# Kernel optimization log

Hardware: AMD Instinct MI355X
Metric: run time of the kernel (lower is better)

The kernel has to match this reference:

```python
import jax, jax.numpy as jnp
import numpy as np

T, B = 128, 32
E, H, V = 512, 1024, 32000


def setup_inputs() -> dict:
    key = jax.random.key(0)
    ks = jax.random.split(key, 9)
    s = 0.02
    return {
        "inputs": jax.random.randint(ks[0], (T, B), 0, V),
        "encoder_output": jax.random.normal(ks[1], (T, B, H), dtype=jnp.float32),
        "encoder_mask": jnp.ones((T, B), dtype=bool),
        "emb": jax.random.normal(ks[2], (V, E), dtype=jnp.float32) * s,
        "w_ih": jax.random.normal(ks[3], (3 * H, E), dtype=jnp.float32) * s,
        "w_hh": jax.random.normal(ks[4], (3 * H, H), dtype=jnp.float32) * s,
        "b_ih": jax.random.normal(ks[5], (3 * H,), dtype=jnp.float32) * s,
        "b_hh": jax.random.normal(ks[6], (3 * H,), dtype=jnp.float32) * s,
        "out_w": jax.random.normal(ks[7], (V, H), dtype=jnp.float32) * s,
        "out_b": jax.random.normal(ks[8], (V,), dtype=jnp.float32) * s,
    }


def reference(inputs, encoder_output, encoder_mask, emb, w_ih, w_hh, b_ih, b_hh, out_w, out_b):
    # Eval-mode (teacher-forced) semantics of the loop: the GRU consumes
    # [inputs[0], inputs[0], inputs[1], ..., inputs[T-2]].
    x_idx = jnp.concatenate([inputs[:1], inputs[:-1]], axis=0)        # [T,B]
    x = emb[x_idx]                                                    # [T,B,E]
    # Precompute input-side gate pre-activations for all steps (big GEMM).
    gx = jnp.einsum('tbe,ge->tbg', x, w_ih) + b_ih                    # [T,B,3H]

    def step(h, gx_t):
        gh = h @ w_hh.T + b_hh                                        # [B,3H]
        xr, xz, xn = jnp.split(gx_t, 3, axis=-1)
        hr, hz, hn = jnp.split(gh, 3, axis=-1)
        r = jax.nn.sigmoid(xr + hr)
        z = jax.nn.sigmoid(xz + hz)
        n = jnp.tanh(xn + r * hn)
        h_new = (1.0 - z) * n + z * h
        return h_new, h_new

    h0 = jnp.zeros((B, H), dtype=x.dtype)
    h_last, outputs = jax.lax.scan(step, h0, gx)                      # [T,B,H]
    logits = jnp.einsum('tbh,vh->tbv', outputs, out_w) + out_b        # [T,B,V]
    return logits, h_last[None]                                       # hidden: [num_layers,B,H]
```

## Files before the change

### kernel.cpp

```cpp
#include <hip/hip_runtime.h>
#include <hip/hip_bf16.h>
#include <stdint.h>

#define TT 128
#define BB 32
#define EE 512
#define HH 1024
#define VV 32000

typedef unsigned short u16;
typedef short bf16x8 __attribute__((ext_vector_type(8)));
typedef float f32x4 __attribute__((ext_vector_type(4)));

__device__ __forceinline__ u16 f2bf(float f) {
    unsigned int u = __builtin_bit_cast(unsigned int, f);
    u = (u + 0x7fffu + ((u >> 16) & 1u)) >> 16;
    return (u16)u;
}

__device__ __forceinline__ void gld_lds16(const u16* g, u16* l) {
    __builtin_amdgcn_global_load_lds(
        (__attribute__((address_space(1))) void*)g,
        (__attribute__((address_space(3))) void*)l, 16, 0, 0);
}

__global__ void k_cast(const float* __restrict__ s, u16* __restrict__ d, int n4) {
    int i = blockIdx.x * blockDim.x + threadIdx.x;
    if (i < n4) {
        float4 v = ((const float4*)s)[i];
        ushort4 o = { f2bf(v.x), f2bf(v.y), f2bf(v.z), f2bf(v.w) };
        ((ushort4*)d)[i] = o;
    }
}

__global__ void k_embed(const int* __restrict__ inp, const float* __restrict__ emb,
                        u16* __restrict__ x) {
    int row = blockIdx.x;
    int t = row >> 5, b = row & 31;
    int st = (t == 0) ? 0 : (t - 1);
    int idx = inp[st * BB + b];
    int e = threadIdx.x * 4;
    float4 v = *(const float4*)(emb + (size_t)idx * EE + e);
    ushort4 o = { f2bf(v.x), f2bf(v.y), f2bf(v.z), f2bf(v.w) };
    *(ushort4*)(x + (size_t)row * EE + e) = o;
}

__global__ __launch_bounds__(256) void k_gemm_bt(
    const u16* __restrict__ A, const u16* __restrict__ B,
    const float* __restrict__ bias, float* __restrict__ C,
    int M, int N, int K)
{
    __shared__ u16 As[128 * 32];
    __shared__ u16 Bs[128 * 32];
    const int tid  = threadIdx.x;
    const int wave = tid >> 6;
    const int lane = tid & 63;
    const int m0 = blockIdx.y * 128;
    const int n0 = blockIdx.x * 128;
    const int wm = wave & 1;
    const int wn = wave >> 1;

    f32x4 acc[4][4];
    #pragma unroll
    for (int i = 0; i < 4; ++i)
        #pragma unroll
        for (int j = 0; j < 4; ++j) {
            f32x4 z = {0.f, 0.f, 0.f, 0.f};
            acc[i][j] = z;
        }

    const int srow = tid >> 2;
    const int scol = (tid & 3) * 8;
    const int mrow = wm * 64 + (lane & 15);
    const int nrow = wn * 64 + (lane & 15);
    const int kq   = (lane >> 4) * 8;

    for (int k0 = 0; k0 < K; k0 += 32) {
        __syncthreads();
        #pragma unroll
        for (int i = 0; i < 2; ++i) {
            int row = i * 64 + srow;
            gld_lds16(A + (size_t)(m0 + row) * K + k0 + scol,
                      As + (size_t)(i * 256 + wave * 64) * 8);
            gld_lds16(B + (size_t)(n0 + row) * K + k0 + scol,
                      Bs + (size_t)(i * 256 + wave * 64) * 8);
        }
        __syncthreads();

        bf16x8 a[4], b[4];
        #pragma unroll
        for (int x = 0; x < 4; ++x) {
            a[x] = *(const bf16x8*)&As[(mrow + x * 16) * 32 + kq];
            b[x] = *(const bf16x8*)&Bs[(nrow + x * 16) * 32 + kq];
        }
        #pragma unroll
        for (int mi = 0; mi < 4; ++mi)
            #pragma unroll
            for (int ni = 0; ni < 4; ++ni)
                acc[mi][ni] = __builtin_amdgcn_mfma_f32_16x16x32_bf16(
                    a[mi], b[ni], acc[mi][ni], 0, 0, 0);
    }

    const int rbase = m0 + wm * 64 + (lane >> 4) * 4;
    const int cbase = n0 + wn * 64 + (lane & 15);
    #pragma unroll
    for (int mi = 0; mi < 4; ++mi) {
        #pragma unroll
        for (int ni = 0; ni < 4; ++ni) {
            int c = cbase + ni * 16;
            float bv = bias[c];
            int r0 = rbase + mi * 16;
            #pragma unroll
            for (int rr = 0; rr < 4; ++rr)
                C[(size_t)(r0 + rr) * N + c] = acc[mi][ni][rr] + bv;
        }
    }
}

__global__ __launch_bounds__(192) void k_gru_step(
    const float* __restrict__ gxt,
    const u16*   __restrict__ hprev_bf,
    const float* __restrict__ hprev_f,
    const u16*   __restrict__ whh,
    const float* __restrict__ bhh,
    float* __restrict__ hout_f,
    u16*   __restrict__ hout_bf)
{
    __shared__ float gh[3][2][16][16];
    const int tid  = threadIdx.x;
    const int wave = tid >> 6;
    const int lane = tid & 63;
    const int j0   = blockIdx.x * 16;
    const int c16  = lane & 15;
    const int kq   = (lane >> 4) * 8;

    f32x4 acc0 = {0.f, 0.f, 0.f, 0.f};
    f32x4 acc1 = {0.f, 0.f, 0.f, 0.f};
    const u16* brow  = whh + (size_t)(wave * HH + j0 + c16) * HH;
    const u16* arow0 = hprev_bf + (size_t)c16 * HH;
    const u16* arow1 = hprev_bf + (size_t)(16 + c16) * HH;

    for (int kk = 0; kk < HH; kk += 32) {
        bf16x8 b  = *(const bf16x8*)&brow[kk + kq];
        bf16x8 a0 = *(const bf16x8*)&arow0[kk + kq];
        bf16x8 a1 = *(const bf16x8*)&arow1[kk + kq];
        acc0 = __builtin_amdgcn_mfma_f32_16x16x32_bf16(a0, b, acc0, 0, 0, 0);
        acc1 = __builtin_amdgcn_mfma_f32_16x16x32_bf16(a1, b, acc1, 0, 0, 0);
    }

    #pragma unroll
    for (int rr = 0; rr < 4; ++rr) {
        gh[wave][0][(lane >> 4) * 4 + rr][c16] = acc0[rr];
        gh[wave][1][(lane >> 4) * 4 + rr][c16] = acc1[rr];
    }
    __syncthreads();

    for (int e = tid; e < BB * 16; e += 192) {
        int row = e >> 4, col = e & 15;
        int j = j0 + col;
        int m = row >> 4, rl = row & 15;
        float hr = gh[0][m][rl][col] + bhh[j];
        float hz = gh[1][m][rl][col] + bhh[HH + j];
        float hn = gh[2][m][rl][col] + bhh[2 * HH + j];
        const float* gxrow = gxt + (size_t)row * (3 * HH);
        float r = 1.f / (1.f + expf(-(gxrow[j] + hr)));
        float z = 1.f / (1.f + expf(-(gxrow[HH + j] + hz)));
        float n = tanhf(gxrow[2 * HH + j] + r * hn);
        float hnew = (1.f - z) * n + z * hprev_f[(size_t)row * HH + j];
        hout_f[(size_t)row * HH + j] = hnew;
        hout_bf[(size_t)row * HH + j] = f2bf(hnew);
    }
}

extern "C" void kernel_launch(void* const* d_in, const int* in_sizes, int n_in,
                              void* d_out, int out_size, void* d_ws, size_t ws_size,
                              hipStream_t stream) {
    const int*   inputs = (const int*)d_in[0];
    const float* emb    = (const float*)d_in[3];
    const float* w_ih   = (const float*)d_in[4];
    const float* w_hh   = (const float*)d_in[5];
    const float* b_ih   = (const float*)d_in[6];
    const float* b_hh   = (const float*)d_in[7];
    const float* out_w  = (const float*)d_in[8];
    const float* out_b  = (const float*)d_in[9];
    float* out = (float*)d_out;

    char* ws = (char*)d_ws;
    u16*   wih_bf  = (u16*)  (ws + 0);
    u16*   whh_bf  = (u16*)  (ws + 3145728);
    u16*   outw_bf = (u16*)  (ws + 9437184);
    u16*   x_bf    = (u16*)  (ws + 74973184);
    float* gx      = (float*)(ws + 79167488);
    u16*   hseq    = (u16*)  (ws + 129499136);
    u16*   hz_bf   = (u16*)  (ws + 137887744);
    float* h0      = (float*)(ws + 137953280);
    float* h1      = (float*)(ws + 138084352);
    float* hbuf[2] = { h0, h1 };

    k_cast<<<1536,  256, 0, stream>>>(w_ih,  wih_bf,  (3*HH*EE)/4);
    k_cast<<<3072,  256, 0, stream>>>(w_hh,  whh_bf,  (3*HH*HH)/4);
    k_cast<<<32000, 256, 0, stream>>>(out_w, outw_bf, ((size_t)VV*HH)/4);
    k_embed<<<TT*BB, 128, 0, stream>>>(inputs, emb, x_bf);
    {
        dim3 g(3*HH/128, (TT*BB)/128);
        k_gemm_bt<<<g, 256, 0, stream>>>(x_bf, wih_bf, b_ih, gx, TT*BB, 3*HH, EE);
    }
    hipMemsetAsync(h0, 0, BB*HH*sizeof(float), stream);
    hipMemsetAsync(hz_bf, 0, BB*HH*sizeof(u16), stream);
    for (int t = 0; t < TT; ++t) {
        const u16*   hb = (t == 0) ? hz_bf : hseq + (size_t)(t-1)*BB*HH;
        const float* hf = hbuf[t & 1];
        float*       ho = hbuf[(t + 1) & 1];
        k_gru_step<<<HH/16, 192, 0, stream>>>(gx + (size_t)t*BB*3*HH, hb, hf,
                                              whh_bf, b_hh, ho,
                                              hseq + (size_t)t*BB*HH);
    }
    {
        dim3 g(VV/128, (TT*BB)/128);
        k_gemm_bt<<<g, 256, 0, stream>>>(hseq, outw_bf, out_b, out, TT*BB, VV, HH);
    }
    hipMemcpyAsync(out + (size_t)TT*BB*VV, hbuf[0], BB*HH*sizeof(float),
                   hipMemcpyDeviceToDevice, stream);
}
```

Before: 2.714 ms.

## Replace per-step GRU launches with persistent cooperative kernel holding W_hh in LDS

Replaces the 128 per-timestep kernel launches with a single cooperative kernel of 64 blocks that loops over all timesteps and uses grid.sync between steps. Each block converts its 48-row slice of W_hh to bf16 once and keeps it in LDS, so the weights are not re-read from global memory every step. The fp32 hidden state also stays in LDS, and the final state is written straight to the output, which removes the separate W_hh cast kernel, a memset and the final copy. In exchange it depends on cooperative launch with all 64 blocks co-resident, and each step pays a grid-wide barrier.

```diff
diff --git a/kernel.cpp b/kernel.cpp
--- a/kernel.cpp
+++ b/kernel.cpp
@@ -1,6 +1,9 @@
 #include <hip/hip_runtime.h>
+#include <hip/hip_cooperative_groups.h>
 #include <hip/hip_bf16.h>
 #include <stdint.h>
+
+namespace cg = cooperative_groups;
 
 #define TT 128
 #define BB 32
@@ -117,16 +120,19 @@
     }
 }
 
-__global__ __launch_bounds__(192) void k_gru_step(
-    const float* __restrict__ gxt,
-    const u16*   __restrict__ hprev_bf,
-    const float* __restrict__ hprev_f,
-    const u16*   __restrict__ whh,
+__global__ __launch_bounds__(192) void k_gru_scan(
+    const float* __restrict__ gx,
+    const u16*   __restrict__ hz,
+    const float* __restrict__ whh,
     const float* __restrict__ bhh,
-    float* __restrict__ hout_f,
-    u16*   __restrict__ hout_bf)
+    u16*   __restrict__ hseq,
+    float* __restrict__ hfin)
 {
+    __shared__ u16   wl[48][1032];
     __shared__ float gh[3][2][16][16];
+    __shared__ float hf[32][16];
+
+    cg::grid_group grid = cg::this_grid();
     const int tid  = threadIdx.x;
     const int wave = tid >> 6;
     const int lane = tid & 63;
@@ -134,41 +140,85 @@
     const int c16  = lane & 15;
     const int kq   = (lane >> 4) * 8;
 
-    f32x4 acc0 = {0.f, 0.f, 0.f, 0.f};
-    f32x4 acc1 = {0.f, 0.f, 0.f, 0.f};
-    const u16* brow  = whh + (size_t)(wave * HH + j0 + c16) * HH;
-    const u16* arow0 = hprev_bf + (size_t)c16 * HH;
-    const u16* arow1 = hprev_bf + (size_t)(16 + c16) * HH;
-
-    for (int kk = 0; kk < HH; kk += 32) {
-        bf16x8 b  = *(const bf16x8*)&brow[kk + kq];
-        bf16x8 a0 = *(const bf16x8*)&arow0[kk + kq];
-        bf16x8 a1 = *(const bf16x8*)&arow1[kk + kq];
-        acc0 = __builtin_amdgcn_mfma_f32_16x16x32_bf16(a0, b, acc0, 0, 0, 0);
-        acc1 = __builtin_amdgcn_mfma_f32_16x16x32_bf16(a1, b, acc1, 0, 0, 0);
-    }
-
+    for (int i = tid; i < 48 * 128; i += 192) {
+        int lr = i >> 7;
+        int e8 = (i & 127) << 3;
+        const float* src = whh + (size_t)((lr >> 4) * HH + j0 + (lr & 15)) * HH + e8;
+        float4 v0 = *(const float4*)src;
+        float4 v1 = *(const float4*)(src + 4);
+        bf16x8 o;
+        o[0] = (short)f2bf(v0.x); o[1] = (short)f2bf(v0.y);
+        o[2] = (short)f2bf(v0.z); o[3] = (short)f2bf(v0.w);
+        o[4] = (short)f2bf(v1.x); o[5] = (short)f2bf(v1.y);
+        o[6] = (short)f2bf(v1.z); o[7] = (short)f2bf(v1.w);
+        *(bf16x8*)&wl[lr][e8] = o;
+    }
+    for (int i = tid; i < 512; i += 192) hf[i >> 4][i & 15] = 0.f;
+    float br_[3], bz_[3], bn_[3];
     #pragma unroll
-    for (int rr = 0; rr < 4; ++rr) {
-        gh[wave][0][(lane >> 4) * 4 + rr][c16] = acc0[rr];
-        gh[wave][1][(lane >> 4) * 4 + rr][c16] = acc1[rr];
+    for (int i = 0; i < 3; ++i) {
+        int e = tid + 192 * i;
+        if (e < 512) {
+            int j = j0 + (e & 15);
+            br_[i] = bhh[j]; bz_[i] = bhh[HH + j]; bn_[i] = bhh[2 * HH + j];
+        }
     }
     __syncthreads();
 
-    for (int e = tid; e < BB * 16; e += 192) {
-        int row = e >> 4, col = e & 15;
-        int j = j0 + col;
-        int m = row >> 4, rl = row & 15;
-        float hr = gh[0][m][rl][col] + bhh[j];
-        float hz = gh[1][m][rl][col] + bhh[HH + j];
-        float hn = gh[2][m][rl][col] + bhh[2 * HH + j];
-        const float* gxrow = gxt + (size_t)row * (3 * HH);
-        float r = 1.f / (1.f + expf(-(gxrow[j] + hr)));
-        float z = 1.f / (1.f + expf(-(gxrow[HH + j] + hz)));
-        float n = tanhf(gxrow[2 * HH + j] + r * hn);
-        float hnew = (1.f - z) * n + z * hprev_f[(size_t)row * HH + j];
-        hout_f[(size_t)row * HH + j] = hnew;
-        hout_bf[(size_t)row * HH + j] = f2bf(hnew);
+    const u16* hprev = hz;
+    const int wrow = wave * 16 + c16;
+    for (int t = 0; t < TT; ++t) {
+        float gr_[3], gz_[3], gn_[3];
+        const float* gxt = gx + (size_t)t * (BB * 3 * HH);
+        #pragma unroll
+        for (int i = 0; i < 3; ++i) {
+            int e = tid + 192 * i;
+            if (e < 512) {
+                const float* g = gxt + (size_t)(e >> 4) * (3 * HH) + j0 + (e & 15);
+                gr_[i] = g[0]; gz_[i] = g[HH]; gn_[i] = g[2 * HH];
+            }
+        }
+        f32x4 acc0 = {0.f, 0.f, 0.f, 0.f};
+        f32x4 acc1 = {0.f, 0.f, 0.f, 0.f};
+        const u16* a0p = hprev + (size_t)c16 * HH + kq;
+        const u16* a1p = a0p + (size_t)16 * HH;
+        const u16* blp = &wl[wrow][kq];
+        for (int kk = 0; kk < HH; kk += 32) {
+            bf16x8 b  = *(const bf16x8*)(blp + kk);
+            bf16x8 a0 = *(const bf16x8*)(a0p + kk);
+            bf16x8 a1 = *(const bf16x8*)(a1p + kk);
+            acc0 = __builtin_amdgcn_mfma_f32_16x16x32_bf16(a0, b, acc0, 0, 0, 0);
+            acc1 = __builtin_amdgcn_mfma_f32_16x16x32_bf16(a1, b, acc1, 0, 0, 0);
+        }
+        #pragma unroll
+        for (int rr = 0; rr < 4; ++rr) {
+            gh[wave][0][(lane >> 4) * 4 + rr][c16] = acc0[rr];
+            gh[wave][1][(lane >> 4) * 4 + rr][c16] = acc1[rr];
+        }
+        __syncthreads();
+        u16* hout = hseq + (size_t)t * BB * HH;
+        #pragma unroll
+        for (int i = 0; i < 3; ++i) {
+            int e = tid + 192 * i;
+            if (e < 512) {
+                int row = e >> 4, col = e & 15;
+                float hr  = gh[0][row >> 4][row & 15][col] + br_[i];
+                float hz_ = gh[1][row >> 4][row & 15][col] + bz_[i];
+                float hn  = gh[2][row >> 4][row & 15][col] + bn_[i];
+                float r = 1.f / (1.f + expf(-(gr_[i] + hr)));
+                float z = 1.f / (1.f + expf(-(gz_[i] + hz_)));
+                float n = tanhf(gn_[i] + r * hn);
+                float hnew = (1.f - z) * n + z * hf[row][col];
+                hf[row][col] = hnew;
+                hout[(size_t)row * HH + j0 + col] = f2bf(hnew);
+            }
+        }
+        hprev = hout;
+        if (t != TT - 1) grid.sync();
+    }
+    for (int i = tid; i < 512; i += 192) {
+        int row = i >> 4, col = i & 15;
+        hfin[(size_t)row * HH + j0 + col] = hf[row][col];
     }
 }
 
@@ -187,38 +237,34 @@
 
     char* ws = (char*)d_ws;
     u16*   wih_bf  = (u16*)  (ws + 0);
-    u16*   whh_bf  = (u16*)  (ws + 3145728);
     u16*   outw_bf = (u16*)  (ws + 9437184);
     u16*   x_bf    = (u16*)  (ws + 74973184);
     float* gx      = (float*)(ws + 79167488);
     u16*   hseq    = (u16*)  (ws + 129499136);
     u16*   hz_bf   = (u16*)  (ws + 137887744);
-    float* h0      = (float*)(ws + 137953280);
-    float* h1      = (float*)(ws + 138084352);
-    float* hbuf[2] = { h0, h1 };
 
     k_cast<<<1536,  256, 0, stream>>>(w_ih,  wih_bf,  (3*HH*EE)/4);
-    k_cast<<<3072,  256, 0, stream>>>(w_hh,  whh_bf,  (3*HH*HH)/4);
     k_cast<<<32000, 256, 0, stream>>>(out_w, outw_bf, ((size_t)VV*HH)/4);
     k_embed<<<TT*BB, 128, 0, stream>>>(inputs, emb, x_bf);
     {
         dim3 g(3*HH/128, (TT*BB)/128);
         k_gemm_bt<<<g, 256, 0, stream>>>(x_bf, wih_bf, b_ih, gx, TT*BB, 3*HH, EE);
     }
-    hipMemsetAsync(h0, 0, BB*HH*sizeof(float), stream);
     hipMemsetAsync(hz_bf, 0, BB*HH*sizeof(u16), stream);
-    for (int t = 0; t < TT; ++t) {
-        const u16*   hb = (t == 0) ? hz_bf : hseq + (size_t)(t-1)*BB*HH;
-        const float* hf = hbuf[t & 1];
-        float*       ho = hbuf[(t + 1) & 1];
-        k_gru_step<<<HH/16, 192, 0, stream>>>(gx + (size_t)t*BB*3*HH, hb, hf,
-                                              whh_bf, b_hh, ho,
-                                              hseq + (size_t)t*BB*HH);
+    {
+        const float* gxp  = gx;
+        const u16*   hzp  = hz_bf;
+        const float* whhp = w_hh;
+        const float* bhhp = b_hh;
+        u16*         hsp  = hseq;
+        float*       hfp  = out + (size_t)TT * BB * VV;
+        void* args[] = { (void*)&gxp, (void*)&hzp, (void*)&whhp,
+                         (void*)&bhhp, (void*)&hsp, (void*)&hfp };
+        hipLaunchCooperativeKernel((const void*)k_gru_scan, dim3(64), dim3(192),
+                                   args, 0, stream);
     }
     {
         dim3 g(VV/128, (TT*BB)/128);
         k_gemm_bt<<<g, 256, 0, stream>>>(hseq, outw_bf, out_b, out, TT*BB, VV, HH);
     }
-    hipMemcpyAsync(out + (size_t)TT*BB*VV, hbuf[0], BB*HH*sizeof(float),
-                   hipMemcpyDeviceToDevice, stream);
-}
+}
```

Measured after the change: 2.966 ms. 1.09x slower.
